# Optimization experiments

Measured on AMD Instinct MI355X. Metric: run time of the kernel, lower is better.

## Reference

```python
import jax, jax.numpy as jnp
import numpy as np

N, E, IN_DIM, H_DIM, T = 100000, 3200000, 128, 128, 5000


def gcn_conv(x, W, b, src, dst):
    """PyG GCNConv: symmetric norm with self-loops, linear transform, scatter-add."""
    n = x.shape[0]
    h = x @ W  # [N, h]
    # degree with self-loops (all edge weights = 1)
    deg = jax.ops.segment_sum(jnp.ones(src.shape[0], x.dtype), dst, num_segments=n) + 1.0
    dinv = jax.lax.rsqrt(deg)  # deg >= 1 due to self-loops
    norm = dinv[src] * dinv[dst]  # [E]
    out = jax.ops.segment_sum(h[src] * norm[:, None], dst, num_segments=n)
    out = out + h * (dinv * dinv)[:, None]  # self-loop contribution
    return out + b


def setup_inputs() -> dict:
    key = jax.random.key(0)
    ks = jax.random.split(key, 24)
    s_in = 1.0 / np.sqrt(IN_DIM)
    s_h = 1.0 / np.sqrt(H_DIM)
    return {
        "x": jax.random.normal(ks[0], (N, IN_DIM), jnp.float32),
        "edge_index": jax.random.randint(ks[1], (2, E), 0, N),
        "fake_x": jax.random.normal(ks[2], (N, IN_DIM), jnp.float32),
        "fake_edge_index": jax.random.randint(ks[3], (2, E), 0, N),
        "treat_idx": jax.random.randint(ks[4], (T,), 0, N),
        "control_idx": jax.random.randint(ks[5], (T,), 0, N),
        # GCN layer params
        "W1": jax.random.normal(ks[6], (IN_DIM, H_DIM), jnp.float32) * s_in,
        "b1": jnp.zeros((H_DIM,), jnp.float32),
        "W2": jax.random.normal(ks[7], (H_DIM, H_DIM), jnp.float32) * s_h,
        "b2": jnp.zeros((H_DIM,), jnp.float32),
        # heads
        "Wy1": jax.random.normal(ks[8], (H_DIM, 1), jnp.float32) * s_h,
        "by1": jnp.zeros((1,), jnp.float32),
        "Wy0": jax.random.normal(ks[9], (H_DIM, 1), jnp.float32) * s_h,
        "by0": jnp.zeros((1,), jnp.float32),
        "Wb": jax.random.normal(ks[10], (H_DIM, 2), jnp.float32) * s_h,
        "bb": jnp.zeros((2,), jnp.float32),
        "Wp1": jax.random.normal(ks[11], (H_DIM, H_DIM), jnp.float32) * s_h,
        "bp1": jnp.zeros((H_DIM,), jnp.float32),
        "Wp2": jax.random.normal(ks[12], (H_DIM, 2), jnp.float32) * s_h,
        "bp2": jnp.zeros((2,), jnp.float32),
    }


@jax.custom_vjp
def grl(x):
    return x

def _grl_fwd(x):
    return x, None

def _grl_bwd(_, g):
    return (-g,)

grl.defvjp(_grl_fwd, _grl_bwd)


def reference(x, edge_index, fake_x, fake_edge_index, treat_idx, control_idx,
              W1, b1, W2, b2, Wy1, by1, Wy0, by0, Wb, bb, Wp1, bp1, Wp2, bp2):
    lrelu = jax.nn.leaky_relu  # slope 0.01 matches torch default
    src, dst = edge_index[0], edge_index[1]
    fsrc, fdst = fake_edge_index[0], fake_edge_index[1]

    # layer 1 + relu (dropout is identity in eval mode)
    xZ1 = jax.nn.relu(gcn_conv(x, W1, b1, src, dst))
    xfZ1 = jax.nn.relu(gcn_conv(fake_x, W1, b1, fsrc, fdst))
    # layer 2
    xZ2 = gcn_conv(xZ1, W2, b2, src, dst)
    xfZ2 = gcn_conv(xfZ1, W2, b2, fsrc, fdst)

    y1 = lrelu(xZ2[treat_idx] @ Wy1 + by1).squeeze(-1)
    yc0 = lrelu(xfZ2[treat_idx] @ Wy0 + by0).squeeze(-1)
    y0 = lrelu(xZ2[control_idx] @ Wy0 + by0).squeeze(-1)
    yc1 = lrelu(xfZ2[control_idx] @ Wy1 + by1).squeeze(-1)

    fprob = grl(xZ2) @ Wb + bb
    fprob_f = grl(xfZ2) @ Wb + bb

    tprob = lrelu(lrelu(xZ2 @ Wp1 + bp1) @ Wp2 + bp2)
    tprob_f = lrelu(lrelu(xfZ2 @ Wp1 + bp1) @ Wp2 + bp2)

    return (y1, yc0, y0, yc1, fprob, fprob_f, tprob, tprob_f)
```

## Files before the change

### kernel.cpp

```cpp
#include <hip/hip_runtime.h>

#define DIM 128
#define EPB 8192
#define BINSH 8
#define BINN 256

typedef unsigned int uint32;
typedef __attribute__((ext_vector_type(8))) short short8;
typedef __attribute__((ext_vector_type(4))) float f32x4;

__device__ __forceinline__ uint32 bf16_rtne(float f) {
  uint32 u = __float_as_uint(f);
  return (u + 0x7FFFu + ((u >> 16) & 1u)) >> 16;
}
__device__ __forceinline__ float bf16_to_f(uint32 h) { return __uint_as_float(h << 16); }
__device__ __forceinline__ void unpack2(uint32 u, float& x, float& y) {
  x = __uint_as_float(u << 16);
  y = __uint_as_float(u & 0xFFFF0000u);
}


__launch_bounds__(256)
__global__ void csr_sort_kernel(const int* __restrict__ src, const int* __restrict__ dst,
                                int E, int nb1, uint32* __restrict__ tmp,
                                int* __restrict__ dir) {
  __shared__ uint32 sorted[EPB];
  __shared__ int lcnt[512];
  __shared__ int lbase[512];
  __shared__ int ps[256];
  int t = threadIdx.x;
  int base = blockIdx.x * EPB;

  lcnt[t] = 0;
  lcnt[t + 256] = 0;
  __syncthreads();

  uint32 val[32];
  uint32 br[32];
#pragma unroll
  for (int i = 0; i < 32; ++i) {
    int e = base + i * 256 + t;
    if (e < E) {
      int d = __builtin_nontemporal_load(dst + e);
      int s = __builtin_nontemporal_load(src + e);
      int bin = d >> BINSH;
      val[i] = ((uint32)s << BINSH) | (uint32)(d & (BINN - 1));
      int rank = atomicAdd(&lcnt[bin], 1);
      br[i] = ((uint32)bin << 13) | (uint32)rank;
    } else {
      br[i] = 0xFFFFFFFFu;
    }
  }
  __syncthreads();

  {
    int a0 = lcnt[2 * t], a1 = lcnt[2 * t + 1];
    int psum = a0 + a1;
    ps[t] = psum;
    __syncthreads();
    for (int off = 1; off < 256; off <<= 1) {
      int x = (t >= off) ? ps[t - off] : 0;
      __syncthreads();
      ps[t] += x;
      __syncthreads();
    }
    int ebase = ps[t] - psum;
    lbase[2 * t] = ebase;
    lbase[2 * t + 1] = ebase + a0;
  }
  __syncthreads();

#pragma unroll
  for (int i = 0; i < 32; ++i) {
    if (br[i] != 0xFFFFFFFFu) {
      int bin = br[i] >> 13;
      int rank = br[i] & 0x1FFF;
      sorted[lbase[bin] + rank] = val[i];
    }
  }
  __syncthreads();

  int cnt = min(EPB, E - base);
#pragma unroll
  for (int i = 0; i < 32; ++i) {
    int idx = i * 256 + t;
    if (idx < cnt) tmp[base + idx] = sorted[idx];
  }
  for (int b = t; b <= nb1; b += 256) {
    dir[blockIdx.x * (nb1 + 1) + b] = lbase[b];
  }
}


__launch_bounds__(256)
__global__ void csr_build_kernel(const uint32* __restrict__ tmp, const int* __restrict__ dir,
                                 int nA, int nb1, int N, int binCap,
                                 int* __restrict__ row_beg, int* __restrict__ row_end,
                                 int* __restrict__ cols, float* __restrict__ dinv) {
  __shared__ int rbeg[512];
  __shared__ int rend[512];
  __shared__ int deg[BINN];
  __shared__ int cur[BINN];
  __shared__ int ps[256];
  int j = blockIdx.x;
  int t = threadIdx.x;
  int node0 = j << BINSH;
  int colsBase = j * binCap;

  if (t < BINN) deg[t] = 0;
  for (int i = t; i < nA; i += 256) {
    rbeg[i] = dir[i * (nb1 + 1) + j];
    rend[i] = dir[i * (nb1 + 1) + j + 1];
  }
  __syncthreads();

  for (int i = t; i < nA; i += 256) {
    const uint32* p = tmp + (size_t)i * EPB;
    int b = rbeg[i], en = rend[i];
    for (int q = b; q < en; ++q) {
      atomicAdd(&deg[tmp[(size_t)i * EPB + q] & (BINN - 1)], 1);
    }
    (void)p;
  }
  __syncthreads();

  int dv = deg[t];
  ps[t] = dv;
  __syncthreads();
  for (int off = 1; off < 256; off <<= 1) {
    int x = (t >= off) ? ps[t - off] : 0;
    __syncthreads();
    ps[t] += x;
    __syncthreads();
  }
  int ebase = ps[t] - dv;
  cur[t] = ebase;
  int node = node0 + t;
  if (node < N) {
    row_beg[node] = colsBase + ebase;
    row_end[node] = colsBase + ebase + dv;
    dinv[node] = rsqrtf((float)dv + 1.0f);
  }
  __syncthreads();

  for (int i = t; i < nA; i += 256) {
    int b = rbeg[i], en = rend[i];
    for (int q = b; q < en; ++q) {
      uint32 v = tmp[(size_t)i * EPB + q];
      int p = atomicAdd(&cur[v & (BINN - 1)], 1);
      cols[colsBase + p] = (int)(v >> BINSH);
    }
  }
}


__global__ void wsplit_kernel(const float* __restrict__ W, uint4* __restrict__ hi4,
                              uint4* __restrict__ lo4) {
  int tid = blockIdx.x * blockDim.x + threadIdx.x;
  int lane = tid & 63;
  int ks = (tid >> 6) & 3;
  int ct = tid >> 8;
  int col = ct * 16 + (lane & 15);
  int k0 = ks * 32 + ((lane >> 4) << 3);
  uint32 h[8], l[8];
#pragma unroll
  for (int j = 0; j < 8; ++j) {
    float w = W[(size_t)(k0 + j) * DIM + col];
    uint32 hh = bf16_rtne(w);
    float rem = w - bf16_to_f(hh);
    l[j] = bf16_rtne(rem);
    h[j] = hh;
  }
  uint4 H, L;
  H.x = h[0] | (h[1] << 16); H.y = h[2] | (h[3] << 16);
  H.z = h[4] | (h[5] << 16); H.w = h[6] | (h[7] << 16);
  L.x = l[0] | (l[1] << 16); L.y = l[2] | (l[3] << 16);
  L.z = l[4] | (l[5] << 16); L.w = l[6] | (l[7] << 16);
  hi4[tid] = H;
  lo4[tid] = L;
}


__launch_bounds__(256, 3)
__global__ void gemm_mfma_kernel(const float* __restrict__ in, const uint4* __restrict__ wHi,
                                 const uint4* __restrict__ wLo, uint32* __restrict__ outb,
                                 int n, const float* __restrict__ rowscale,
                                 const float* __restrict__ bias, float slope) {
  __shared__ unsigned short sA[2 * 64 * 128];
  __shared__ unsigned short sO[64 * 128];
  int t = threadIdx.x;
  int row0 = blockIdx.x * 64;

  {
    int quad = t & 31;
    int r = t >> 5;
#pragma unroll
    for (int i = 0; i < 8; ++i) {
      int row = r + i * 8;
      int grow = row0 + row;
      f32x4 v = (f32x4){0.f, 0.f, 0.f, 0.f};
      if (grow < n) v = *(const f32x4*)(in + (size_t)grow * DIM + quad * 4);
      uint32 h0 = bf16_rtne(v.x), h1 = bf16_rtne(v.y), h2 = bf16_rtne(v.z), h3 = bf16_rtne(v.w);
      uint32 l0 = bf16_rtne(v.x - bf16_to_f(h0));
      uint32 l1 = bf16_rtne(v.y - bf16_to_f(h1));
      uint32 l2 = bf16_rtne(v.z - bf16_to_f(h2));
      uint32 l3 = bf16_rtne(v.w - bf16_to_f(h3));
      int sidx = (row * 128 + quad * 4) ^ ((row & 7) << 3);
      *(uint2*)&sA[sidx] = make_uint2(h0 | (h1 << 16), h2 | (h3 << 16));
      *(uint2*)&sA[64 * 128 + sidx] = make_uint2(l0 | (l1 << 16), l2 | (l3 << 16));
    }
  }
  __syncthreads();

  int lane = t & 63;
  int w = t >> 6;
  int rbase = w * 16;
  f32x4 acc[8];
#pragma unroll
  for (int ct = 0; ct < 8; ++ct) acc[ct] = (f32x4){0.f, 0.f, 0.f, 0.f};

  int fragRow = rbase + (lane & 15);
  int fragSwz = (fragRow & 7) << 3;
#pragma unroll
  for (int ks = 0; ks < 4; ++ks) {
    int cidx = ks * 32 + ((lane >> 4) << 3);
    int sidx = (fragRow * 128 + cidx) ^ fragSwz;
    uint4 au = *(uint4*)&sA[sidx];
    uint4 alu = *(uint4*)&sA[64 * 128 + sidx];
    short8 ah = __builtin_bit_cast(short8, au);
    short8 al = __builtin_bit_cast(short8, alu);
#pragma unroll
    for (int ct = 0; ct < 8; ++ct) {
      int widx = (ct * 4 + ks) * 64 + lane;
      short8 bh = __builtin_bit_cast(short8, wHi[widx]);
      short8 bl = __builtin_bit_cast(short8, wLo[widx]);
      acc[ct] = __builtin_amdgcn_mfma_f32_16x16x32_bf16(al, bh, acc[ct], 0, 0, 0);
      acc[ct] = __builtin_amdgcn_mfma_f32_16x16x32_bf16(ah, bl, acc[ct], 0, 0, 0);
      acc[ct] = __builtin_amdgcn_mfma_f32_16x16x32_bf16(ah, bh, acc[ct], 0, 0, 0);
    }
  }

  float rs[4];
#pragma unroll
  for (int r = 0; r < 4; ++r) {
    int grow = row0 + rbase + ((lane >> 4) << 2) + r;
    rs[r] = rowscale ? ((grow < n) ? rowscale[grow] : 0.f) : 1.0f;
  }
#pragma unroll
  for (int ct = 0; ct < 8; ++ct) {
    int col = ct * 16 + (lane & 15);
    float bv = bias ? bias[col] : 0.f;
#pragma unroll
    for (int r = 0; r < 4; ++r) {
      int rowL = rbase + ((lane >> 4) << 2) + r;
      float v = acc[ct][r] * rs[r] + bv;
      v = (v > 0.f) ? v : v * slope;
      int sidx = (rowL * 128 + col) ^ ((rowL & 7) << 3);
      sO[sidx] = (unsigned short)bf16_rtne(v);
    }
  }
  __syncthreads();
#pragma unroll
  for (int it = 0; it < 4; ++it) {
    int s = it * 64 + lane;
    int row = rbase + (s >> 4);
    int sin = s & 15;
    int sidx = row * 128 + ((sin * 8) ^ ((row & 7) << 3));
    uint4 v = *(uint4*)&sO[sidx];
    int grow = row0 + row;
    if (grow < n) *(uint4*)(outb + (size_t)grow * 64 + sin * 4) = v;
  }
}


__launch_bounds__(256)
__global__ void agg_kernel(const uint32* __restrict__ g, const int* __restrict__ row_beg,
                           const int* __restrict__ row_end, const int* __restrict__ cols,
                           const float* __restrict__ dinv, const float* __restrict__ bias,
                           float* __restrict__ out, int n, int relu) {
  int lane = threadIdx.x & 63;
  int node = (blockIdx.x * blockDim.x + threadIdx.x) >> 6;
  if (node >= n) return;
  int beg = row_beg[node];
  int end = row_end[node];
  float ax, ay;
  unpack2(g[(size_t)node * 64 + lane], ax, ay);
  float bx = 0.f, by = 0.f;
  int e = beg;
  for (; e + 8 <= end; e += 8) {
    int s0 = cols[e + 0], s1 = cols[e + 1], s2 = cols[e + 2], s3 = cols[e + 3];
    int s4 = cols[e + 4], s5 = cols[e + 5], s6 = cols[e + 6], s7 = cols[e + 7];
    uint32 u0 = g[(size_t)s0 * 64 + lane];
    uint32 u1 = g[(size_t)s1 * 64 + lane];
    uint32 u2 = g[(size_t)s2 * 64 + lane];
    uint32 u3 = g[(size_t)s3 * 64 + lane];
    uint32 u4 = g[(size_t)s4 * 64 + lane];
    uint32 u5 = g[(size_t)s5 * 64 + lane];
    uint32 u6 = g[(size_t)s6 * 64 + lane];
    uint32 u7 = g[(size_t)s7 * 64 + lane];
    float x0, y0, x1, y1, x2, y2, x3, y3, x4, y4, x5, y5, x6, y6, x7, y7;
    unpack2(u0, x0, y0); unpack2(u1, x1, y1);
    unpack2(u2, x2, y2); unpack2(u3, x3, y3);
    unpack2(u4, x4, y4); unpack2(u5, x5, y5);
    unpack2(u6, x6, y6); unpack2(u7, x7, y7);
    ax += (x0 + x1) + (x2 + x3);
    ay += (y0 + y1) + (y2 + y3);
    bx += (x4 + x5) + (x6 + x7);
    by += (y4 + y5) + (y6 + y7);
  }
  for (; e < end; ++e) {
    uint32 u0 = g[(size_t)cols[e] * 64 + lane];
    float x0, y0;
    unpack2(u0, x0, y0);
    ax += x0;
    ay += y0;
  }
  ax += bx;
  ay += by;
  float di = dinv[node];
  float2 bv = ((const float2*)bias)[lane];
  float ox = fmaf(di, ax, bv.x);
  float oy = fmaf(di, ay, bv.y);
  if (relu) {
    ox = fmaxf(ox, 0.f);
    oy = fmaxf(oy, 0.f);
  }
  ((float2*)out)[(size_t)node * 64 + lane] = make_float2(ox, oy);
}


__global__ void twocol_f32_kernel(const float* __restrict__ Z, const float* __restrict__ Wc,
                                  const float* __restrict__ bc, float* __restrict__ out,
                                  int n, float slope) {
  int lane = threadIdx.x & 63;
  int wid = (blockIdx.x * blockDim.x + threadIdx.x) >> 6;
  int nw = (gridDim.x * blockDim.x) >> 6;
  float w00 = Wc[(2 * lane) * 2 + 0];
  float w01 = Wc[(2 * lane) * 2 + 1];
  float w10 = Wc[(2 * lane + 1) * 2 + 0];
  float w11 = Wc[(2 * lane + 1) * 2 + 1];
  float b0 = bc[0], b1 = bc[1];
  for (int i = wid; i < n; i += nw) {
    float2 z = ((const float2*)Z)[(size_t)i * 64 + lane];
    float p0 = z.x * w00 + z.y * w10;
    float p1 = z.x * w01 + z.y * w11;
#pragma unroll
    for (int off = 32; off; off >>= 1) {
      p0 += __shfl_xor(p0, off);
      p1 += __shfl_xor(p1, off);
    }
    if (lane == 0) {
      float o0 = p0 + b0, o1 = p1 + b1;
      out[2 * (size_t)i + 0] = (o0 > 0.f) ? o0 : slope * o0;
      out[2 * (size_t)i + 1] = (o1 > 0.f) ? o1 : slope * o1;
    }
  }
}

__global__ void twocol_bf16_kernel(const uint32* __restrict__ Z, const float* __restrict__ Wc,
                                   const float* __restrict__ bc, float* __restrict__ out,
                                   int n, float slope) {
  int lane = threadIdx.x & 63;
  int wid = (blockIdx.x * blockDim.x + threadIdx.x) >> 6;
  int nw = (gridDim.x * blockDim.x) >> 6;
  float w00 = Wc[(2 * lane) * 2 + 0];
  float w01 = Wc[(2 * lane) * 2 + 1];
  float w10 = Wc[(2 * lane + 1) * 2 + 0];
  float w11 = Wc[(2 * lane + 1) * 2 + 1];
  float b0 = bc[0], b1 = bc[1];
  for (int i = wid; i < n; i += nw) {
    float zx, zy;
    unpack2(Z[(size_t)i * 64 + lane], zx, zy);
    float p0 = zx * w00 + zy * w10;
    float p1 = zx * w01 + zy * w11;
#pragma unroll
    for (int off = 32; off; off >>= 1) {
      p0 += __shfl_xor(p0, off);
      p1 += __shfl_xor(p1, off);
    }
    if (lane == 0) {
      float o0 = p0 + b0, o1 = p1 + b1;
      out[2 * (size_t)i + 0] = (o0 > 0.f) ? o0 : slope * o0;
      out[2 * (size_t)i + 1] = (o1 > 0.f) ? o1 : slope * o1;
    }
  }
}

__global__ void ydot_kernel(const float* __restrict__ Z, const int* __restrict__ idx,
                            const float* __restrict__ w, const float* __restrict__ b,
                            float* __restrict__ out, int T) {
  int lane = threadIdx.x & 63;
  int t = (blockIdx.x * blockDim.x + threadIdx.x) >> 6;
  if (t >= T) return;
  float2 wv = ((const float2*)w)[lane];
  int node = idx[t];
  float2 z = ((const float2*)Z)[(size_t)node * 64 + lane];
  float pp = z.x * wv.x + z.y * wv.y;
#pragma unroll
  for (int off = 32; off; off >>= 1) pp += __shfl_xor(pp, off);
  if (lane == 0) {
    float o = pp + b[0];
    out[t] = (o > 0.f) ? o : 0.01f * o;
  }
}


extern "C" void kernel_launch(void* const* d_in, const int* in_sizes, int n_in,
                              void* d_out, int out_size, void* d_ws, size_t ws_size,
                              hipStream_t stream) {
  const int N = in_sizes[0] / DIM;
  const int E = in_sizes[1] / 2;
  const int T = in_sizes[4];
  const int nb1 = (N + BINN - 1) >> BINSH;
  const int nA = (E + EPB - 1) / EPB;
  const int binCap = ((E / nb1 + 1024 + 15) / 16) * 16;

  const float* x = (const float*)d_in[0];
  const int* ei = (const int*)d_in[1];
  const float* fx = (const float*)d_in[2];
  const int* fei = (const int*)d_in[3];
  const int* treat = (const int*)d_in[4];
  const int* control = (const int*)d_in[5];
  const float* W1 = (const float*)d_in[6];
  const float* b1 = (const float*)d_in[7];
  const float* W2 = (const float*)d_in[8];
  const float* b2 = (const float*)d_in[9];
  const float* Wy1 = (const float*)d_in[10];
  const float* by1 = (const float*)d_in[11];
  const float* Wy0 = (const float*)d_in[12];
  const float* by0 = (const float*)d_in[13];
  const float* Wb = (const float*)d_in[14];
  const float* bb = (const float*)d_in[15];
  const float* Wp1 = (const float*)d_in[16];
  const float* bp1 = (const float*)d_in[17];
  const float* Wp2 = (const float*)d_in[18];
  const float* bp2 = (const float*)d_in[19];

  float* out = (float*)d_out;

  char* p = (char*)d_ws;
  float* bufZ = (float*)p;   p += (size_t)N * DIM * sizeof(float);
  uint32* bufG = (uint32*)p; p += (size_t)N * (DIM / 2) * sizeof(uint32);
  int* cols = (int*)p;       p += (size_t)nb1 * binCap * sizeof(int);
  int* dir = (int*)p;        p += (size_t)nA * (nb1 + 1) * sizeof(int);
  int* row_beg = (int*)p;    p += (size_t)(N + 16) * sizeof(int);
  int* row_end = (int*)p;    p += (size_t)(N + 16) * sizeof(int);
  float* dinv = (float*)p;   p += (size_t)(N + 16) * sizeof(float);
  uint4* w1Hi = (uint4*)p;   p += 2048 * sizeof(uint4);
  uint4* w1Lo = (uint4*)p;   p += 2048 * sizeof(uint4);
  uint4* w2Hi = (uint4*)p;   p += 2048 * sizeof(uint4);
  uint4* w2Lo = (uint4*)p;   p += 2048 * sizeof(uint4);
  uint4* wp1Hi = (uint4*)p;  p += 2048 * sizeof(uint4);
  uint4* wp1Lo = (uint4*)p;  p += 2048 * sizeof(uint4);
  uint32* tmp = (uint32*)bufZ;

  float* oy1 = out;
  float* oyc0 = out + T;
  float* oy0 = out + 2 * T;
  float* oyc1 = out + 3 * T;
  float* ofp = out + 4 * T;
  float* ofpf = out + 4 * T + 2 * N;
  float* otp = out + 4 * T + 4 * N;
  float* otpf = out + 4 * T + 6 * N;

  wsplit_kernel<<<8, 256, 0, stream>>>(W1, w1Hi, w1Lo);
  wsplit_kernel<<<8, 256, 0, stream>>>(W2, w2Hi, w2Lo);
  wsplit_kernel<<<8, 256, 0, stream>>>(Wp1, wp1Hi, wp1Lo);

  auto run = [&](const float* X, const int* EI,
                 float* y_t, const float* Wt, const float* bt,
                 float* y_c, const float* Wc, const float* bc,
                 float* fp, float* tp) {
    const int* srcp = EI;
    const int* dstp = EI + E;
    csr_sort_kernel<<<nA, 256, 0, stream>>>(srcp, dstp, E, nb1, tmp, dir);
    csr_build_kernel<<<nb1, 256, 0, stream>>>(tmp, dir, nA, nb1, N, binCap,
                                              row_beg, row_end, cols, dinv);
    gemm_mfma_kernel<<<(N + 63) / 64, 256, 0, stream>>>(X, w1Hi, w1Lo, bufG, N, dinv, nullptr, 1.0f);
    agg_kernel<<<(N + 3) / 4, 256, 0, stream>>>(bufG, row_beg, row_end, cols, dinv, b1, bufZ, N, 1);
    gemm_mfma_kernel<<<(N + 63) / 64, 256, 0, stream>>>(bufZ, w2Hi, w2Lo, bufG, N, dinv, nullptr, 1.0f);
    agg_kernel<<<(N + 3) / 4, 256, 0, stream>>>(bufG, row_beg, row_end, cols, dinv, b2, bufZ, N, 0);
    gemm_mfma_kernel<<<(N + 63) / 64, 256, 0, stream>>>(bufZ, wp1Hi, wp1Lo, bufG, N, nullptr, bp1, 0.01f);
    twocol_bf16_kernel<<<2048, 256, 0, stream>>>(bufG, Wp2, bp2, tp, N, 0.01f);
    twocol_f32_kernel<<<2048, 256, 0, stream>>>(bufZ, Wb, bb, fp, N, 1.0f);
    ydot_kernel<<<(T + 3) / 4, 256, 0, stream>>>(bufZ, treat, Wt, bt, y_t, T);
    ydot_kernel<<<(T + 3) / 4, 256, 0, stream>>>(bufZ, control, Wc, bc, y_c, T);
  };

  run(x, ei, oy1, Wy1, by1, oy0, Wy0, by0, ofp, otp);
  run(fx, fei, oyc0, Wy0, by0, oyc1, Wy1, by1, ofpf, otpf);
}
```

Before: 942.6 us.

## Fuse prediction heads into GEMM and aggregation epilogues

```diff
diff --git a/kernel.cpp b/kernel.cpp
--- a/kernel.cpp
+++ b/kernel.cpp
@@ -115,12 +115,10 @@
   __syncthreads();
 
   for (int i = t; i < nA; i += 256) {
-    const uint32* p = tmp + (size_t)i * EPB;
     int b = rbeg[i], en = rend[i];
     for (int q = b; q < en; ++q) {
       atomicAdd(&deg[tmp[(size_t)i * EPB + q] & (BINN - 1)], 1);
     }
-    (void)p;
   }
   __syncthreads();
 
@@ -185,7 +183,10 @@
 __global__ void gemm_mfma_kernel(const float* __restrict__ in, const uint4* __restrict__ wHi,
                                  const uint4* __restrict__ wLo, uint32* __restrict__ outb,
                                  int n, const float* __restrict__ rowscale,
-                                 const float* __restrict__ bias, float slope) {
+                                 const float* __restrict__ bias, float slope,
+                                 const float* __restrict__ headW,
+                                 const float* __restrict__ headB,
+                                 float* __restrict__ headOut) {
   __shared__ unsigned short sA[2 * 64 * 128];
   __shared__ unsigned short sO[64 * 128];
   int t = threadIdx.x;
@@ -246,29 +247,68 @@
     int grow = row0 + rbase + ((lane >> 4) << 2) + r;
     rs[r] = rowscale ? ((grow < n) ? rowscale[grow] : 0.f) : 1.0f;
   }
+
+  float hp0[4] = {0.f, 0.f, 0.f, 0.f};
+  float hp1[4] = {0.f, 0.f, 0.f, 0.f};
+
 #pragma unroll
   for (int ct = 0; ct < 8; ++ct) {
     int col = ct * 16 + (lane & 15);
     float bv = bias ? bias[col] : 0.f;
+    float hw0 = 0.f, hw1 = 0.f;
+    if (headOut) {
+      hw0 = headW[col * 2 + 0];
+      hw1 = headW[col * 2 + 1];
+    }
 #pragma unroll
     for (int r = 0; r < 4; ++r) {
       int rowL = rbase + ((lane >> 4) << 2) + r;
       float v = acc[ct][r] * rs[r] + bv;
       v = (v > 0.f) ? v : v * slope;
-      int sidx = (rowL * 128 + col) ^ ((rowL & 7) << 3);
-      sO[sidx] = (unsigned short)bf16_rtne(v);
-    }
-  }
-  __syncthreads();
-#pragma unroll
-  for (int it = 0; it < 4; ++it) {
-    int s = it * 64 + lane;
-    int row = rbase + (s >> 4);
-    int sin = s & 15;
-    int sidx = row * 128 + ((sin * 8) ^ ((row & 7) << 3));
-    uint4 v = *(uint4*)&sO[sidx];
-    int grow = row0 + row;
-    if (grow < n) *(uint4*)(outb + (size_t)grow * 64 + sin * 4) = v;
+      if (outb) {
+        int sidx = (rowL * 128 + col) ^ ((rowL & 7) << 3);
+        sO[sidx] = (unsigned short)bf16_rtne(v);
+      }
+      if (headOut) {
+        hp0[r] = fmaf(v, hw0, hp0[r]);
+        hp1[r] = fmaf(v, hw1, hp1[r]);
+      }
+    }
+  }
+
+  if (headOut) {
+    float hb0 = headB[0], hb1 = headB[1];
+#pragma unroll
+    for (int r = 0; r < 4; ++r) {
+      float a = hp0[r], b = hp1[r];
+#pragma unroll
+      for (int off = 8; off; off >>= 1) {
+        a += __shfl_xor(a, off);
+        b += __shfl_xor(b, off);
+      }
+      if ((lane & 15) == 0) {
+        int grow = row0 + rbase + ((lane >> 4) << 2) + r;
+        if (grow < n) {
+          float o0 = a + hb0, o1 = b + hb1;
+          headOut[2 * (size_t)grow + 0] = (o0 > 0.f) ? o0 : 0.01f * o0;
+          headOut[2 * (size_t)grow + 1] = (o1 > 0.f) ? o1 : 0.01f * o1;
+        }
+      }
+    }
+  }
+
+  if (outb) {
+    __syncthreads();
+#pragma unroll
+    for (int it = 0; it < 4; ++it) {
+      int s = it * 64 + lane;
+      int row = rbase + (s >> 4);
+      int sin = s & 15;
+      int sidx = row * 128 + ((sin * 8) ^ ((row & 7) << 3));
+      uint4 v = *(uint4*)&sO[sidx];
+      int grow = row0 + row;
+      if (grow < n) *(uint4*)(outb + (size_t)grow * 64 + sin * 4) = v;
+    }
   }
 }
 
@@ -277,7 +317,9 @@
 __global__ void agg_kernel(const uint32* __restrict__ g, const int* __restrict__ row_beg,
                            const int* __restrict__ row_end, const int* __restrict__ cols,
                            const float* __restrict__ dinv, const float* __restrict__ bias,
-                           float* __restrict__ out, int n, int relu) {
+                           float* __restrict__ out, int n, int relu,
+                           const float* __restrict__ fpW, const float* __restrict__ fpB,
+                           float* __restrict__ fpOut) {
   int lane = threadIdx.x & 63;
   int node = (blockIdx.x * blockDim.x + threadIdx.x) >> 6;
   if (node >= n) return;
@@ -326,65 +368,26 @@
     oy = fmaxf(oy, 0.f);
   }
   ((float2*)out)[(size_t)node * 64 + lane] = make_float2(ox, oy);
-}
-
-
-__global__ void twocol_f32_kernel(const float* __restrict__ Z, const float* __restrict__ Wc,
-                                  const float* __restrict__ bc, float* __restrict__ out,
-                                  int n, float slope) {
-  int lane = threadIdx.x & 63;
-  int wid = (blockIdx.x * blockDim.x + threadIdx.x) >> 6;
-  int nw = (gridDim.x * blockDim.x) >> 6;
-  float w00 = Wc[(2 * lane) * 2 + 0];
-  float w01 = Wc[(2 * lane) * 2 + 1];
-  float w10 = Wc[(2 * lane + 1) * 2 + 0];
-  float w11 = Wc[(2 * lane + 1) * 2 + 1];
-  float b0 = bc[0], b1 = bc[1];
-  for (int i = wid; i < n; i += nw) {
-    float2 z = ((const float2*)Z)[(size_t)i * 64 + lane];
-    float p0 = z.x * w00 + z.y * w10;
-    float p1 = z.x * w01 + z.y * w11;
+
+  if (fpOut) {
+    float w00 = fpW[(2 * lane) * 2 + 0];
+    float w01 = fpW[(2 * lane) * 2 + 1];
+    float w10 = fpW[(2 * lane + 1) * 2 + 0];
+    float w11 = fpW[(2 * lane + 1) * 2 + 1];
+    float p0 = ox * w00 + oy * w10;
+    float p1 = ox * w01 + oy * w11;
 #pragma unroll
     for (int off = 32; off; off >>= 1) {
       p0 += __shfl_xor(p0, off);
       p1 += __shfl_xor(p1, off);
     }
     if (lane == 0) {
-      float o0 = p0 + b0, o1 = p1 + b1;
-      out[2 * (size_t)i + 0] = (o0 > 0.f) ? o0 : slope * o0;
-      out[2 * (size_t)i + 1] = (o1 > 0.f) ? o1 : slope * o1;
-    }
-  }
-}
-
-__global__ void twocol_bf16_kernel(const uint32* __restrict__ Z, const float* __restrict__ Wc,
-                                   const float* __restrict__ bc, float* __restrict__ out,
-                                   int n, float slope) {
-  int lane = threadIdx.x & 63;
-  int wid = (blockIdx.x * blockDim.x + threadIdx.x) >> 6;
-  int nw = (gridDim.x * blockDim.x) >> 6;
-  float w00 = Wc[(2 * lane) * 2 + 0];
-  float w01 = Wc[(2 * lane) * 2 + 1];
-  float w10 = Wc[(2 * lane + 1) * 2 + 0];
-  float w11 = Wc[(2 * lane + 1) * 2 + 1];
-  float b0 = bc[0], b1 = bc[1];
-  for (int i = wid; i < n; i += nw) {
-    float zx, zy;
-    unpack2(Z[(size_t)i * 64 + lane], zx, zy);
-    float p0 = zx * w00 + zy * w10;
-    float p1 = zx * w01 + zy * w11;
-#pragma unroll
-    for (int off = 32; off; off >>= 1) {
-      p0 += __shfl_xor(p0, off);
-      p1 += __shfl_xor(p1, off);
-    }
-    if (lane == 0) {
-      float o0 = p0 + b0, o1 = p1 + b1;
-      out[2 * (size_t)i + 0] = (o0 > 0.f) ? o0 : slope * o0;
-      out[2 * (size_t)i + 1] = (o1 > 0.f) ? o1 : slope * o1;
-    }
-  }
-}
+      fpOut[2 * (size_t)node + 0] = p0 + fpB[0];
+      fpOut[2 * (size_t)node + 1] = p1 + fpB[1];
+    }
+  }
+}
+
 
 __global__ void ydot_kernel(const float* __restrict__ Z, const int* __restrict__ idx,
                             const float* __restrict__ w, const float* __restrict__ b,
@@ -476,13 +479,16 @@
     csr_sort_kernel<<<nA, 256, 0, stream>>>(srcp, dstp, E, nb1, tmp, dir);
     csr_build_kernel<<<nb1, 256, 0, stream>>>(tmp, dir, nA, nb1, N, binCap,
                                               row_beg, row_end, cols, dinv);
-    gemm_mfma_kernel<<<(N + 63) / 64, 256, 0, stream>>>(X, w1Hi, w1Lo, bufG, N, dinv, nullptr, 1.0f);
-    agg_kernel<<<(N + 3) / 4, 256, 0, stream>>>(bufG, row_beg, row_end, cols, dinv, b1, bufZ, N, 1);
-    gemm_mfma_kernel<<<(N + 63) / 64, 256, 0, stream>>>(bufZ, w2Hi, w2Lo, bufG, N, dinv, nullptr, 1.0f);
-    agg_kernel<<<(N + 3) / 4, 256, 0, stream>>>(bufG, row_beg, row_end, cols, dinv, b2, bufZ, N, 0);
-    gemm_mfma_kernel<<<(N + 63) / 64, 256, 0, stream>>>(bufZ, wp1Hi, wp1Lo, bufG, N, nullptr, bp1, 0.01f);
-    twocol_bf16_kernel<<<2048, 256, 0, stream>>>(bufG, Wp2, bp2, tp, N, 0.01f);
-    twocol_f32_kernel<<<2048, 256, 0, stream>>>(bufZ, Wb, bb, fp, N, 1.0f);
+    gemm_mfma_kernel<<<(N + 63) / 64, 256, 0, stream>>>(X, w1Hi, w1Lo, bufG, N, dinv,
+                                                        nullptr, 1.0f, nullptr, nullptr, nullptr);
+    agg_kernel<<<(N + 3) / 4, 256, 0, stream>>>(bufG, row_beg, row_end, cols, dinv, b1,
+                                                bufZ, N, 1, nullptr, nullptr, nullptr);
+    gemm_mfma_kernel<<<(N + 63) / 64, 256, 0, stream>>>(bufZ, w2Hi, w2Lo, bufG, N, dinv,
+                                                        nullptr, 1.0f, nullptr, nullptr, nullptr);
+    agg_kernel<<<(N + 3) / 4, 256, 0, stream>>>(bufG, row_beg, row_end, cols, dinv, b2,
+                                                bufZ, N, 0, Wb, bb, fp);
+    gemm_mfma_kernel<<<(N + 63) / 64, 256, 0, stream>>>(bufZ, wp1Hi, wp1Lo, nullptr, N, nullptr,
+                                                        bp1, 0.01f, Wp2, bp2, tp);
     ydot_kernel<<<(T + 3) / 4, 256, 0, stream>>>(bufZ, treat, Wt, bt, y_t, T);
     ydot_kernel<<<(T + 3) / 4, 256, 0, stream>>>(bufZ, control, Wc, bc, y_c, T);
   };
```

Result: faster. 888.5 us (-5.7%).
